# Kernel tuning notes

Measured on AMD Instinct MI355X. Metric: run time of the kernel, lower is better.

## Reference

```python
import jax, jax.numpy as jnp
import numpy as np

B, S, H = 4, 2048, 1024
NH, HD = 16, 64
ROPE_THETA = 160000.0
SCALE = HD ** -0.5


def _rope_cos_sin(position_ids, dim, theta):
    # neox-style rotary: frequencies over half the head dim
    inv_freq = 1.0 / (theta ** (jnp.arange(0, dim, 2, dtype=jnp.float32) / dim))  # [dim/2]
    freqs = position_ids.astype(jnp.float32)[..., None] * inv_freq  # [B,S,dim/2]
    return jnp.cos(freqs), jnp.sin(freqs)


def _apply_rope(x, cos, sin):
    # x: [B,S,NH,HD]; neox style: rotate halves
    d2 = x.shape[-1] // 2
    x1, x2 = x[..., :d2], x[..., d2:]
    c = cos[:, :, None, :]
    s = sin[:, :, None, :]
    return jnp.concatenate([x1 * c - x2 * s, x2 * c + x1 * s], axis=-1)


def setup_inputs() -> dict:
    key = jax.random.key(0)
    k1, k2, k3 = jax.random.split(key, 3)
    hidden_states = jax.random.normal(k1, (B, S, H), dtype=jnp.float32)
    position_ids = jnp.tile(jnp.arange(S, dtype=jnp.int32)[None, :], (B, 1))
    Wqkv = jax.random.normal(k2, (3 * H, H), dtype=jnp.float32) * (H ** -0.5)
    Wo = jax.random.normal(k3, (H, H), dtype=jnp.float32) * (H ** -0.5)
    return {"hidden_states": hidden_states, "position_ids": position_ids,
            "Wqkv": Wqkv, "Wo": Wo}


def reference(hidden_states, position_ids, Wqkv, Wo):
    # fused QKV projection
    qkv = jnp.einsum('bsh,oh->bso', hidden_states, Wqkv)  # [B,S,3H]
    q, k, v = jnp.split(qkv, 3, axis=-1)
    q = q.reshape(B, S, NH, HD)
    k = k.reshape(B, S, NH, HD)
    v = v.reshape(B, S, NH, HD)
    # rotary embedding (neox style)
    cos, sin = _rope_cos_sin(position_ids, HD, ROPE_THETA)
    q = _apply_rope(q, cos, sin)
    k = _apply_rope(k, cos, sin)
    # full bidirectional (encoder-only, global layer) attention
    scores = jnp.einsum('bqhd,bkhd->bhqk', q, k) * SCALE  # [B,NH,S,S]
    probs = jax.nn.softmax(scores, axis=-1)
    ctx = jnp.einsum('bhqk,bkhd->bqhd', probs, v).reshape(B, S, H)
    # output projection
    return jnp.einsum('bsh,oh->bso', ctx, Wo)
```

## Files before the change

kernel.cpp:

```cpp
#include <hip/hip_runtime.h>
#include <hip/hip_bf16.h>


#define GLOBAL_AS __attribute__((address_space(1)))
#define LDS_AS    __attribute__((address_space(3)))

using f32x4  = __attribute__((ext_vector_type(4))) float;
using f32x16 = __attribute__((ext_vector_type(16))) float;
using s16x8  = __attribute__((ext_vector_type(8))) short;

__device__ __forceinline__ void gld_lds16(const void* g, void* l) {
  __builtin_amdgcn_global_load_lds((const GLOBAL_AS void*)g, (LDS_AS void*)l, 16, 0, 0);
}

__device__ __forceinline__ unsigned short f2bf(float f) {
  unsigned int u = __float_as_uint(f);
  u = (u + 0x7fffu + ((u >> 16) & 1u)) >> 16;
  return (unsigned short)u;
}
__device__ __forceinline__ unsigned int cvt_pk_bf16(float lo, float hi) {
  unsigned int r;
  asm("v_cvt_pk_bf16_f32 %0, %1, %2" : "=v"(r) : "v"(lo), "v"(hi));
  return r;
}
__device__ __forceinline__ void pswap(unsigned int& a, unsigned int& b) {
  asm("v_permlane32_swap_b32 %0, %1" : "+v"(a), "+v"(b));
}

__global__ __launch_bounds__(256) void cvt_all_kernel(const float* __restrict__ h,
                                                      const float* __restrict__ wq,
                                                      const float* __restrict__ wo,
                                                      unsigned short* __restrict__ hb,
                                                      unsigned short* __restrict__ wqb,
                                                      unsigned short* __restrict__ wob) {
  int b = blockIdx.x;
  const float* src; unsigned short* dst; int i;
  if (b < 8192)       { src = h;  dst = hb;  i = b * 256 + threadIdx.x; }
  else if (b < 11264) { src = wq; dst = wqb; i = (b - 8192) * 256 + threadIdx.x; }
  else                { src = wo; dst = wob; i = (b - 11264) * 256 + threadIdx.x; }
  float4 v = ((const float4*)src)[i];
  ushort4 o;
  o.x = f2bf(v.x); o.y = f2bf(v.y); o.z = f2bf(v.z); o.w = f2bf(v.w);
  ((ushort4*)dst)[i] = o;
}

__global__ __launch_bounds__(256) void rope_table_kernel(const int* __restrict__ pos,
                                                         float* __restrict__ ctab,
                                                         float* __restrict__ stab) {
  int idx = blockIdx.x * 256 + threadIdx.x;
  int d = idx & 31;
  int bs = idx >> 5;
  float p = (float)pos[bs];
  float inv = exp2f(-(float)d * 0.5402410118609203f);
  float f = p * inv;
  ctab[idx] = cosf(f);
  stab[idx] = sinf(f);
}

template<int MODE>
__global__ __launch_bounds__(256) void gemm_bt_kernel(const unsigned short* __restrict__ A,
                                                      const unsigned short* __restrict__ Bm,
                                                      void* __restrict__ C, int N, int K,
                                                      const float* __restrict__ ctab,
                                                      const float* __restrict__ stab,
                                                      unsigned short* __restrict__ Qr,
                                                      unsigned short* __restrict__ Kr,
                                                      unsigned short* __restrict__ vbuf) {
  __shared__ char sA[16384];
  __shared__ char sB[16384];
  const int tid  = threadIdx.x;
  const int lane = tid & 63, w = tid >> 6;
  const int g = lane >> 4, c = lane & 15;
  const int wr = w >> 1, wc = w & 1;
  const int m0 = blockIdx.x * 128, n0 = blockIdx.y * 128;
  const char* Ab = (const char*)A;
  const char* Bb = (const char*)Bm;

  f32x4 acc[4][4] = {};
  for (int k0 = 0; k0 < K; k0 += 64) {
    __syncthreads();
#pragma unroll
    for (int rr = 0; rr < 4; ++rr) {
      int o = tid * 16 + rr * 4096;
      int row = o >> 7;
      int col = (o & 127) ^ ((row & 7) << 4);
      gld_lds16(Ab + ((size_t)(m0 + row) * K + k0) * 2 + col, sA + o);
      gld_lds16(Bb + ((size_t)(n0 + row) * K + k0) * 2 + col, sB + o);
    }
    __syncthreads();
#pragma unroll
    for (int ks = 0; ks < 2; ++ks) {
      s16x8 af[4], bfr[4];
#pragma unroll
      for (int i = 0; i < 4; ++i) {
        int row = 64 * wr + 16 * i + c;
        af[i] = *(const s16x8*)(sA + ((row * 128 + ks * 64 + g * 16) ^ ((row & 7) << 4)));
      }
#pragma unroll
      for (int j = 0; j < 4; ++j) {
        int row = 64 * wc + 16 * j + c;
        bfr[j] = *(const s16x8*)(sB + ((row * 128 + ks * 64 + g * 16) ^ ((row & 7) << 4)));
      }
#pragma unroll
      for (int i = 0; i < 4; ++i)
#pragma unroll
        for (int j = 0; j < 4; ++j)
          acc[i][j] = __builtin_amdgcn_mfma_f32_16x16x32_bf16(af[i], bfr[j], acc[i][j], 0, 0, 0);
    }
  }

  if (MODE == 1) {
#pragma unroll
    for (int i = 0; i < 4; ++i)
#pragma unroll
      for (int j = 0; j < 4; ++j)
#pragma unroll
        for (int r = 0; r < 4; ++r) {
          int m = m0 + 64 * wr + 16 * i + 4 * g + r;
          int n = n0 + 64 * wc + 16 * j + c;
          ((float*)C)[(size_t)m * N + n] = acc[i][j][r];
        }
  } else {
    const int t = blockIdx.y;
    if (t < 16) {
      unsigned short* dstb = (t < 8) ? Qr : Kr;
      const float qs = (t < 8) ? 0.18033688011112042f : 1.0f;
      const int h = 2 * (t & 7) + wc;
#pragma unroll
      for (int i = 0; i < 4; ++i)
#pragma unroll
        for (int r = 0; r < 4; ++r) {
          int m = m0 + 64 * wr + 16 * i + 4 * g + r;
          int b = m >> 11, s = m & 2047;
          unsigned short* drow = dstb + ((size_t)(b * 16 + h) * 2048 + s) * 64;
#pragma unroll
          for (int j = 0; j < 2; ++j) {
            int d = 16 * j + c;
            float co = ctab[(size_t)m * 32 + d];
            float si = stab[(size_t)m * 32 + d];
            float x1 = acc[i][j][r], x2 = acc[i][j + 2][r];
            drow[d]      = f2bf((x1 * co - x2 * si) * qs);
            drow[d + 32] = f2bf((x2 * co + x1 * si) * qs);
          }
        }
    } else {
#pragma unroll
      for (int i = 0; i < 4; ++i)
#pragma unroll
        for (int j = 0; j < 4; ++j)
#pragma unroll
          for (int r = 0; r < 4; ++r) {
            int m = m0 + 64 * wr + 16 * i + 4 * g + r;
            int n = (t - 16) * 128 + 64 * wc + 16 * j + c;
            vbuf[(size_t)m * 1024 + n] = f2bf(acc[i][j][r]);
          }
    }
  }
}

__global__ __launch_bounds__(256) void vtrans_kernel(const unsigned short* __restrict__ vbuf,
                                                     unsigned short* __restrict__ Vt) {
  __shared__ unsigned short tile[64][80];
  int bid = blockIdx.x;
  int st = bid & 31, h = (bid >> 5) & 15, b = bid >> 9;
  int s0 = st * 64;
  int t = threadIdx.x;
  {
    int row = t >> 2, part = t & 3;
    const unsigned short* src = vbuf + ((size_t)(b * 2048 + s0 + row)) * 1024 + h * 64 + part * 16;
    uint4 v0 = *(const uint4*)(src);
    uint4 v1 = *(const uint4*)(src + 8);
    *(uint4*)&tile[row][part * 16]     = v0;
    *(uint4*)&tile[row][part * 16 + 8] = v1;
  }
  __syncthreads();
  {
    int d = t >> 2, sp = t & 3;
    unsigned short vals[16];
#pragma unroll
    for (int i = 0; i < 16; ++i) vals[i] = tile[sp * 16 + i][d];
    unsigned short* dst = Vt + ((size_t)(b * 16 + h) * 64 + d) * 2048 + s0 + sp * 16;
    *(uint4*)(dst)     = ((const uint4*)vals)[0];
    *(uint4*)(dst + 8) = ((const uint4*)vals)[1];
  }
}

__global__ __launch_bounds__(512) void attn_kernel(const unsigned short* __restrict__ Q,
                                                   const unsigned short* __restrict__ Kr,
                                                   const unsigned short* __restrict__ Vt,
                                                   unsigned short* __restrict__ Ctx) {
  __shared__ char sK[3][8192];
  __shared__ char sV[3][8192];
  const int tid  = threadIdx.x;
  const int lane = tid & 63, w = tid >> 6;
  const int hi = lane >> 5, ql = lane & 31;
  const int swz = (ql & 7) << 4;
  int lin = blockIdx.x + 8 * blockIdx.y;
  int eff = (lin & 7) * 64 + (lin >> 3);
  const int bh = eff >> 3;
  const int q0 = (eff & 7) * 256;
  const char* kh = (const char*)(Kr + (size_t)bh * 2048 * 64);
  const char* vh = (const char*)(Vt + (size_t)bh * 64 * 2048);

  s16x8 qf[4];
  {
    const char* qrow = (const char*)Q + ((size_t)bh * 2048 + q0 + 32 * w + ql) * 128;
#pragma unroll
    for (int t = 0; t < 4; ++t) qf[t] = *(const s16x8*)(qrow + t * 32 + hi * 16);
  }
  __builtin_amdgcn_sched_barrier(0);

#define STAGE(t, b)                                                              \
  {                                                                              \
    int o = tid * 16;                                                            \
    int l = o ^ (((o >> 7) & 7) << 4);                                           \
    gld_lds16(kh + (size_t)(t) * 8192 + l, sK[b] + o);                           \
    gld_lds16(vh + (size_t)(o >> 7) * 4096 + (t) * 128 + (l & 127), sV[b] + o);  \
  }

  STAGE(0, 0);
  __builtin_amdgcn_sched_barrier(0);
  STAGE(1, 1);
  __builtin_amdgcn_sched_barrier(0);

  float l_run = 0.f;
  f32x16 oa0 = {}, oa1 = {};
  int cur = 0;

  for (int it = 0; it < 32; ++it) {
    if (it == 0 || it == 31) asm volatile("s_waitcnt vmcnt(0)" ::: "memory");
    else                     asm volatile("s_waitcnt vmcnt(2)" ::: "memory");
    __builtin_amdgcn_sched_barrier(0);
    __builtin_amdgcn_s_barrier();
    __builtin_amdgcn_sched_barrier(0);

    if (it + 2 < 32) {
      int sb = cur + 2; if (sb >= 3) sb -= 3;
      STAGE(it + 2, sb);
    }
    __builtin_amdgcn_sched_barrier(0);

    f32x16 sc0 = {}, sc1 = {};
    __builtin_amdgcn_s_setprio(1);
#pragma unroll
    for (int t = 0; t < 4; ++t) {
      int cx = (t * 32 + hi * 16) ^ swz;
      s16x8 k0 = *(const s16x8*)(sK[cur] + ql * 128 + cx);
      s16x8 k1 = *(const s16x8*)(sK[cur] + (32 + ql) * 128 + cx);
      sc0 = __builtin_amdgcn_mfma_f32_32x32x16_bf16(k0, qf[t], sc0, 0, 0, 0);
      sc1 = __builtin_amdgcn_mfma_f32_32x32x16_bf16(k1, qf[t], sc1, 0, 0, 0);
    }
    __builtin_amdgcn_s_setprio(0);

    float rs = 0.f;
#pragma unroll
    for (int r = 0; r < 16; ++r) { sc0[r] = __builtin_amdgcn_exp2f(sc0[r]); rs += sc0[r]; }
#pragma unroll
    for (int r = 0; r < 16; ++r) { sc1[r] = __builtin_amdgcn_exp2f(sc1[r]); rs += sc1[r]; }
    l_run += rs;

    unsigned int bp[16];
#pragma unroll
    for (int blk = 0; blk < 2; ++blk) {
      const f32x16& s = blk ? sc1 : sc0;
      unsigned int a0 = cvt_pk_bf16(s[0],  s[1]);
      unsigned int a1 = cvt_pk_bf16(s[2],  s[3]);
      unsigned int a2 = cvt_pk_bf16(s[4],  s[5]);
      unsigned int a3 = cvt_pk_bf16(s[6],  s[7]);
      pswap(a0, a2); pswap(a1, a3);
      bp[blk * 8 + 0] = a0; bp[blk * 8 + 1] = a1;
      bp[blk * 8 + 2] = a2; bp[blk * 8 + 3] = a3;
      unsigned int b0 = cvt_pk_bf16(s[8],  s[9]);
      unsigned int b1 = cvt_pk_bf16(s[10], s[11]);
      unsigned int b2 = cvt_pk_bf16(s[12], s[13]);
      unsigned int b3 = cvt_pk_bf16(s[14], s[15]);
      pswap(b0, b2); pswap(b1, b3);
      bp[blk * 8 + 4] = b0; bp[blk * 8 + 5] = b1;
      bp[blk * 8 + 6] = b2; bp[blk * 8 + 7] = b3;
    }

    __builtin_amdgcn_s_setprio(1);
#pragma unroll
    for (int ss = 0; ss < 4; ++ss) {
      uint4 u = {bp[ss * 4], bp[ss * 4 + 1], bp[ss * 4 + 2], bp[ss * 4 + 3]};
      s16x8 pb = __builtin_bit_cast(s16x8, u);
      int cx = (ss * 32 + hi * 16) ^ swz;
      s16x8 v0 = *(const s16x8*)(sV[cur] + ql * 128 + cx);
      s16x8 v1 = *(const s16x8*)(sV[cur] + (32 + ql) * 128 + cx);
      oa0 = __builtin_amdgcn_mfma_f32_32x32x16_bf16(v0, pb, oa0, 0, 0, 0);
      oa1 = __builtin_amdgcn_mfma_f32_32x32x16_bf16(v1, pb, oa1, 0, 0, 0);
    }
    __builtin_amdgcn_s_setprio(0);

    ++cur; if (cur == 3) cur = 0;
  }
#undef STAGE

  l_run += __shfl_xor(l_run, 32);
  float inv = 1.f / l_run;
  const int b = bh >> 4, h = bh & 15;
  const int q = q0 + 32 * w + ql;
  unsigned short* crow = Ctx + ((size_t)(b * 2048 + q)) * 1024 + h * 64;
#pragma unroll
  for (int dblk = 0; dblk < 2; ++dblk) {
    const f32x16& oa = dblk ? oa1 : oa0;
#pragma unroll
    for (int grp = 0; grp < 4; ++grp) {
      ushort4 st;
      st.x = f2bf(oa[4 * grp + 0] * inv);
      st.y = f2bf(oa[4 * grp + 1] * inv);
      st.z = f2bf(oa[4 * grp + 2] * inv);
      st.w = f2bf(oa[4 * grp + 3] * inv);
      *(ushort4*)(crow + dblk * 32 + 8 * grp + 4 * hi) = st;
    }
  }
}

extern "C" void kernel_launch(void* const* d_in, const int* in_sizes, int n_in,
                              void* d_out, int out_size, void* d_ws, size_t ws_size,
                              hipStream_t stream) {
  const float* hidden = (const float*)d_in[0];
  const int*   pos    = (const int*)d_in[1];
  const float* wqkv   = (const float*)d_in[2];
  const float* wo     = (const float*)d_in[3];

  char* ws = (char*)d_ws;
  unsigned short* hbf  = (unsigned short*)(ws);
  unsigned short* wqbf = (unsigned short*)(ws + 16777216);
  unsigned short* wobf = (unsigned short*)(ws + 23068672);
  unsigned short* vbuf = (unsigned short*)(ws + 25165824);
  unsigned short* Qr   = (unsigned short*)(ws + 41943040);
  unsigned short* Kr   = (unsigned short*)(ws + 58720256);
  unsigned short* Vt   = (unsigned short*)(ws + 75497472);
  unsigned short* ctx  = (unsigned short*)(ws + 92274688);
  float*          ctab = (float*)(ws + 109051904);
  float*          stab = (float*)(ws + 110100480);

  cvt_all_kernel<<<12288, 256, 0, stream>>>(hidden, wqkv, wo, hbf, wqbf, wobf);
  rope_table_kernel<<<1024, 256, 0, stream>>>(pos, ctab, stab);

  dim3 gq(64, 24);
  gemm_bt_kernel<2><<<gq, 256, 0, stream>>>(hbf, wqbf, nullptr, 3072, 1024,
                                            ctab, stab, Qr, Kr, vbuf);

  vtrans_kernel<<<2048, 256, 0, stream>>>(vbuf, Vt);

  dim3 ga(8, 64);
  attn_kernel<<<ga, 512, 0, stream>>>(Qr, Kr, Vt, ctx);

  dim3 go(64, 8);
  gemm_bt_kernel<1><<<go, 256, 0, stream>>>(ctx, wobf, d_out, 1024, 1024,
                                            nullptr, nullptr, nullptr, nullptr, nullptr);
}
```

Baseline: 193.6 us.

## Fuse V transpose into QKV GEMM epilogue and merge rope table into convert kernel

The QKV GEMM epilogue for V tiles now stages the accumulator tile in shared memory and writes the transposed Vt layout directly, so the intermediate vbuf and the separate vtrans kernel are gone. The rope cos/sin table computation is folded into the fp32-to-bf16 conversion kernel as extra blocks, which saves a launch. Together these remove about 16 MB of global round-trip traffic and two kernel launches. The cost is extra syncthreads and LDS traffic in the GEMM epilogue, and possible LDS bank conflicts from the 74-element row pitch.

```diff
diff --git a/kernel.cpp b/kernel.cpp
--- a/kernel.cpp
+++ b/kernel.cpp
@@ -27,13 +27,27 @@
   asm("v_permlane32_swap_b32 %0, %1" : "+v"(a), "+v"(b));
 }
 
-__global__ __launch_bounds__(256) void cvt_all_kernel(const float* __restrict__ h,
-                                                      const float* __restrict__ wq,
-                                                      const float* __restrict__ wo,
-                                                      unsigned short* __restrict__ hb,
-                                                      unsigned short* __restrict__ wqb,
-                                                      unsigned short* __restrict__ wob) {
+__global__ __launch_bounds__(256) void cvt_rope_kernel(const float* __restrict__ h,
+                                                       const float* __restrict__ wq,
+                                                       const float* __restrict__ wo,
+                                                       const int* __restrict__ pos,
+                                                       unsigned short* __restrict__ hb,
+                                                       unsigned short* __restrict__ wqb,
+                                                       unsigned short* __restrict__ wob,
+                                                       float* __restrict__ ctab,
+                                                       float* __restrict__ stab) {
   int b = blockIdx.x;
+  if (b >= 12288) {
+    int idx = (b - 12288) * 256 + threadIdx.x;
+    int d = idx & 31;
+    int bs = idx >> 5;
+    float p = (float)pos[bs];
+    float inv = exp2f(-(float)d * 0.5402410118609203f);
+    float f = p * inv;
+    ctab[idx] = cosf(f);
+    stab[idx] = sinf(f);
+    return;
+  }
   const float* src; unsigned short* dst; int i;
   if (b < 8192)       { src = h;  dst = hb;  i = b * 256 + threadIdx.x; }
   else if (b < 11264) { src = wq; dst = wqb; i = (b - 8192) * 256 + threadIdx.x; }
@@ -44,19 +58,6 @@
   ((ushort4*)dst)[i] = o;
 }
 
-__global__ __launch_bounds__(256) void rope_table_kernel(const int* __restrict__ pos,
-                                                         float* __restrict__ ctab,
-                                                         float* __restrict__ stab) {
-  int idx = blockIdx.x * 256 + threadIdx.x;
-  int d = idx & 31;
-  int bs = idx >> 5;
-  float p = (float)pos[bs];
-  float inv = exp2f(-(float)d * 0.5402410118609203f);
-  float f = p * inv;
-  ctab[idx] = cosf(f);
-  stab[idx] = sinf(f);
-}
-
 template<int MODE>
 __global__ __launch_bounds__(256) void gemm_bt_kernel(const unsigned short* __restrict__ A,
                                                       const unsigned short* __restrict__ Bm,
@@ -65,9 +66,10 @@
                                                       const float* __restrict__ stab,
                                                       unsigned short* __restrict__ Qr,
                                                       unsigned short* __restrict__ Kr,
-                                                      unsigned short* __restrict__ vbuf) {
-  __shared__ char sA[16384];
-  __shared__ char sB[16384];
+                                                      unsigned short* __restrict__ Vt) {
+  __shared__ char sAB[32768];
+  char* sA = sAB;
+  char* sB = sAB + 16384;
   const int tid  = threadIdx.x;
   const int lane = tid & 63, w = tid >> 6;
   const int g = lane >> 4, c = lane & 15;
@@ -144,44 +146,35 @@
           }
         }
     } else {
-#pragma unroll
-      for (int i = 0; i < 4; ++i)
-#pragma unroll
-        for (int j = 0; j < 4; ++j)
-#pragma unroll
-          for (int r = 0; r < 4; ++r) {
-            int m = m0 + 64 * wr + 16 * i + 4 * g + r;
-            int n = (t - 16) * 128 + 64 * wc + 16 * j + c;
-            vbuf[(size_t)m * 1024 + n] = f2bf(acc[i][j][r]);
-          }
-    }
-  }
-}
-
-__global__ __launch_bounds__(256) void vtrans_kernel(const unsigned short* __restrict__ vbuf,
-                                                     unsigned short* __restrict__ Vt) {
-  __shared__ unsigned short tile[64][80];
-  int bid = blockIdx.x;
-  int st = bid & 31, h = (bid >> 5) & 15, b = bid >> 9;
-  int s0 = st * 64;
-  int t = threadIdx.x;
-  {
-    int row = t >> 2, part = t & 3;
-    const unsigned short* src = vbuf + ((size_t)(b * 2048 + s0 + row)) * 1024 + h * 64 + part * 16;
-    uint4 v0 = *(const uint4*)(src);
-    uint4 v1 = *(const uint4*)(src + 8);
-    *(uint4*)&tile[row][part * 16]     = v0;
-    *(uint4*)&tile[row][part * 16 + 8] = v1;
-  }
-  __syncthreads();
-  {
-    int d = t >> 2, sp = t & 3;
-    unsigned short vals[16];
-#pragma unroll
-    for (int i = 0; i < 16; ++i) vals[i] = tile[sp * 16 + i][d];
-    unsigned short* dst = Vt + ((size_t)(b * 16 + h) * 64 + d) * 2048 + s0 + sp * 16;
-    *(uint4*)(dst)     = ((const uint4*)vals)[0];
-    *(uint4*)(dst + 8) = ((const uint4*)vals)[1];
+      unsigned short (*tile)[74] = (unsigned short (*)[74])sAB;
+      const int bb = m0 >> 11, sb = m0 & 2047;
+#pragma unroll
+      for (int hp = 0; hp < 2; ++hp) {
+        __syncthreads();
+        if (wc == hp) {
+#pragma unroll
+          for (int i = 0; i < 4; ++i)
+#pragma unroll
+            for (int j = 0; j < 4; ++j)
+#pragma unroll
+              for (int r = 0; r < 4; ++r)
+                tile[64 * wr + 16 * i + 4 * g + r][16 * j + c] = f2bf(acc[i][j][r]);
+        }
+        __syncthreads();
+        int h = (t - 16) * 2 + hp;
+        int p = tid & 7;
+#pragma unroll
+        for (int dd = 0; dd < 2; ++dd) {
+          int d = (tid >> 3) + 32 * dd;
+          alignas(16) unsigned short vv[16];
+#pragma unroll
+          for (int i2 = 0; i2 < 16; ++i2) vv[i2] = tile[p * 16 + i2][d];
+          unsigned short* dst = Vt + ((size_t)(bb * 16 + h) * 64 + d) * 2048 + sb + p * 16;
+          *(uint4*)dst       = ((const uint4*)vv)[0];
+          *(uint4*)(dst + 8) = ((const uint4*)vv)[1];
+        }
+      }
+    }
   }
 }
 
@@ -328,7 +321,6 @@
   unsigned short* hbf  = (unsigned short*)(ws);
   unsigned short* wqbf = (unsigned short*)(ws + 16777216);
   unsigned short* wobf = (unsigned short*)(ws + 23068672);
-  unsigned short* vbuf = (unsigned short*)(ws + 25165824);
   unsigned short* Qr   = (unsigned short*)(ws + 41943040);
   unsigned short* Kr   = (unsigned short*)(ws + 58720256);
   unsigned short* Vt   = (unsigned short*)(ws + 75497472);
@@ -336,14 +328,12 @@
   float*          ctab = (float*)(ws + 109051904);
   float*          stab = (float*)(ws + 110100480);
 
-  cvt_all_kernel<<<12288, 256, 0, stream>>>(hidden, wqkv, wo, hbf, wqbf, wobf);
-  rope_table_kernel<<<1024, 256, 0, stream>>>(pos, ctab, stab);
+  cvt_rope_kernel<<<13312, 256, 0, stream>>>(hidden, wqkv, wo, pos,
+                                             hbf, wqbf, wobf, ctab, stab);
 
   dim3 gq(64, 24);
   gemm_bt_kernel<2><<<gq, 256, 0, stream>>>(hbf, wqbf, nullptr, 3072, 1024,
-                                            ctab, stab, Qr, Kr, vbuf);
-
-  vtrans_kernel<<<2048, 256, 0, stream>>>(vbuf, Vt);
+                                            ctab, stab, Qr, Kr, Vt);
 
   dim3 ga(8, 64);
   attn_kernel<<<ga, 512, 0, stream>>>(Qr, Kr, Vt, ctx);
```

Result: faster. 187.9 us (-2.9%).
